# Kernel optimization log

Hardware: AMD Instinct MI355X
Metric: run time of the kernel (lower is better)

Reference implementation:

```python
import jax, jax.numpy as jnp
import numpy as np

N = 524288
MAXV = 8  # rect-rect intersection has at most 8 vertices
EPS = 1e-8


def setup_inputs() -> dict:
    key = jax.random.key(0)
    k1, k2, k3 = jax.random.split(key, 3)
    return {
        "box": jax.random.normal(k1, (N, 11), jnp.float32),
        "box_target": jax.random.normal(k2, (N, 11), jnp.float32),
        "weight": jax.random.uniform(k3, (N, 11), jnp.float32),
        "avg_factor": N // 2,
    }


def decode_box(box):
    # [x,y,z,logW,logL,logH,sin,cos,v...] -> [x,y,z,W,L,H,yaw,v...]
    yaw = jnp.arctan2(box[..., 6], box[..., 7])
    return jnp.concatenate(
        [box[..., :3], jnp.exp(box[..., 3:6]), yaw[..., None], box[..., 8:]], axis=-1)


def get_rect_vertices(bev):
    # bev: (5,) = [cx, cy, w, l, yaw] -> (4, 2) corners, CCW, rotated about center
    cx, cy, w, l, yaw = bev[0], bev[1], bev[2], bev[3], bev[4]
    dx, dy = w / 2, l / 2
    lx = jnp.stack([-dx, dx, dx, -dx])
    ly = jnp.stack([-dy, -dy, dy, dy])
    s, c = jnp.sin(yaw), jnp.cos(yaw)
    return jnp.stack([lx * c - ly * s + cx, lx * s + ly * c + cy], axis=-1)


def clip_halfplane(poly, count, a, b):
    # Sutherland-Hodgman clip of poly (MAXV,2) with `count` valid verts
    # against left side of directed edge a->b. Fixed-size buffer + mask.
    d = b - a  # (2,)
    idx = jnp.arange(MAXV)
    cnt = jnp.maximum(count, 1)
    prev = poly[(idx - 1) % cnt]
    cur = poly

    def is_left(p):
        return d[0] * (p[..., 1] - a[1]) - d[1] * (p[..., 0] - a[0]) >= 0

    cur_in, prev_in = is_left(cur), is_left(prev)
    num = (a[0] - prev[:, 0]) * d[1] - (a[1] - prev[:, 1]) * d[0]
    den = (cur[:, 0] - prev[:, 0]) * d[1] - (cur[:, 1] - prev[:, 1]) * d[0] + EPS
    ip = prev + (num / den)[:, None] * (cur - prev)  # edge/halfplane intersection
    valid = idx < count
    emit_ip = valid & (prev_in ^ cur_in)   # crossing edge -> emit intersection
    emit_cur = valid & cur_in              # inside vertex -> emit it
    # interleave per-input-edge outputs in original order (ip, then cur)
    pts = jnp.stack([ip, cur], axis=1).reshape(2 * MAXV, 2)
    emit = jnp.stack([emit_ip, emit_cur], axis=1).reshape(2 * MAXV)
    pos = jnp.where(emit, jnp.cumsum(emit) - 1, MAXV)  # compact valid pts to front
    out = jnp.zeros((MAXV, 2), poly.dtype).at[pos].set(
        jnp.where(emit[:, None], pts, 0.0), mode="drop")
    return out, jnp.minimum(emit.sum(), MAXV).astype(jnp.int32)


def poly_area(poly, count):
    # shoelace over the `count` valid vertices
    idx = jnp.arange(MAXV)
    nxt = poly[(idx + 1) % jnp.maximum(count, 1)]
    cross = jnp.where(idx < count, poly[:, 0] * nxt[:, 1] - poly[:, 1] * nxt[:, 0], 0.0)
    return jnp.abs(cross.sum() / 2.0)


def giou_one(bev1, bev2):
    v1 = get_rect_vertices(bev1)  # (4,2)
    v2 = get_rect_vertices(bev2)
    poly = jnp.zeros((MAXV, 2), bev1.dtype).at[:4].set(v1)
    count = jnp.int32(4)
    for i in range(4):  # clip subject rect by 4 half-planes of clip rect
        poly, count = clip_halfplane(poly, count, v2[i], v2[(i + 1) % 4])
        count = jnp.where(count < 3, 0, count)  # degenerate -> empty (original break)
    inter = poly_area(poly, count)
    area1 = bev1[2] * bev1[3]
    area2 = bev2[2] * bev2[3]
    union = area1 + area2 - inter
    allp = jnp.concatenate([v1, v2], axis=0)
    enclosing = (allp[:, 0].max() - allp[:, 0].min()) * (allp[:, 1].max() - allp[:, 1].min())
    iou = inter / (union + EPS)
    return iou - (enclosing - union) / (enclosing + EPS)


def _bev(dec):
    return jnp.stack([dec[:, 0], dec[:, 1], dec[:, 3], dec[:, 4], dec[:, 6]], axis=-1)


def reference(box, box_target, weight, avg_factor):
    af = max(float(avg_factor), 1.0)
    # L1 box loss (reg_weights are all 1.0 per init defaults)
    loss_box = (jnp.abs(box - box_target) * weight).sum() / af
    # rotated BEV GIoU loss
    bev_p = _bev(decode_box(box))
    bev_t = _bev(decode_box(box_target))
    giou = jax.vmap(giou_one)(bev_p, bev_t)
    loss_giou = (1.0 - giou).sum() / af
    return loss_box, loss_giou
```

## Files before the change

### kernel.cpp

```cpp
#include <hip/hip_runtime.h>

#define BLOCK 256
#define ITERS 2
#define EPSF 1e-8f

#define CHUNKS 176

struct Nine { float4 b0, b1, b2, t0, t1, t2, w0, w1, w2; };

__device__ __forceinline__ long lmin(long a, long b) { return a < b ? a : b; }

__device__ __forceinline__ float l1c(float4 b, float4 t, float4 w) {
    return fabsf(b.x - t.x) * w.x + fabsf(b.y - t.y) * w.y +
           fabsf(b.z - t.z) * w.z + fabsf(b.w - t.w) * w.w;
}

__device__ __forceinline__ float safe_rcp(float d) {
    float sd = (fabsf(d) > 1e-30f) ? d : copysignf(1e-30f, d);
    return __frcp_rn(sd);
}

__device__ __forceinline__ float clip_len(float px, float py,
                                          float rdx, float rdy,
                                          float hx, float hy) {
    float t1x = (-hx - px) * rdx, t2x = (hx - px) * rdx;
    float t1y = (-hy - py) * rdy, t2y = (hy - py) * rdy;
    float tmin = fmaxf(fmaxf(fminf(t1x, t2x), fminf(t1y, t2y)), 0.f);
    float tmax = fminf(fminf(fmaxf(t1x, t2x), fmaxf(t1y, t2y)), 1.f);
    return fmaxf(tmax - tmin, 0.f);
}

__device__ __forceinline__ float giou_term(
    float cx1, float cy1, float lw1, float ll1, float sy1, float cw1,
    float cx2, float cy2, float lw2, float ll2, float sy2, float cw2)
{
    float w1v = __expf(lw1), l1v = __expf(ll1);
    float w2v = __expf(lw2), l2v = __expf(ll2);
    float r1 = rsqrtf(fmaxf(sy1 * sy1 + cw1 * cw1, 1e-30f));
    float s1 = sy1 * r1, c1 = cw1 * r1;
    float r2 = rsqrtf(fmaxf(sy2 * sy2 + cw2 * cw2, 1e-30f));
    float s2 = sy2 * r2, c2 = cw2 * r2;

    float hx1 = 0.5f * w1v, hy1 = 0.5f * l1v;
    float hx2 = 0.5f * w2v, hy2 = 0.5f * l2v;

    float e1x = fabsf(hx1 * c1) + fabsf(hy1 * s1);
    float e1y = fabsf(hx1 * s1) + fabsf(hy1 * c1);
    float e2x = fabsf(hx2 * c2) + fabsf(hy2 * s2);
    float e2y = fabsf(hx2 * s2) + fabsf(hy2 * c2);
    float enc = (fmaxf(cx1 + e1x, cx2 + e2x) - fminf(cx1 - e1x, cx2 - e2x))
              * (fmaxf(cy1 + e1y, cy2 + e2y) - fminf(cy1 - e1y, cy2 - e2y));

    float dxw = cx1 - cx2, dyw = cy1 - cy2;
    float txl =  c2 * dxw + s2 * dyw;
    float tyl = -s2 * dxw + c2 * dyw;
    float cr_ = c1 * c2 + s1 * s2;
    float sr_ = s1 * c2 - c1 * s2;

    float ax_ = hx1 * cr_, ay_ = hx1 * sr_;
    float bx_ = hy1 * sr_, by_ = hy1 * cr_;
    float q0x = txl - ax_ + bx_, q0y = tyl - ay_ - by_;
    float q1x = txl + ax_ + bx_, q1y = tyl + ay_ - by_;
    float q2x = txl + ax_ - bx_, q2y = tyl + ay_ + by_;
    float q3x = txl - ax_ - bx_, q3y = tyl - ay_ + by_;

    float inter2 = 0.f;
    {
        float d01x = 2.f * ax_, d01y = 2.f * ay_;
        float d12x = -2.f * bx_, d12y = 2.f * by_;
        float r01x = safe_rcp(d01x), r01y = safe_rcp(d01y);
        float r12x = safe_rcp(d12x), r12y = safe_rcp(d12y);
        float L0 = clip_len(q0x, q0y,  r01x,  r01y, hx2, hy2);
        inter2 += L0 * (q0x * d01y - q0y * d01x);
        float L1 = clip_len(q1x, q1y,  r12x,  r12y, hx2, hy2);
        inter2 += L1 * (q1x * d12y - q1y * d12x);
        float L2 = clip_len(q2x, q2y, -r01x, -r01y, hx2, hy2);
        inter2 += L2 * (q2y * d01x - q2x * d01y);
        float L3 = clip_len(q3x, q3y, -r12x, -r12y, hx2, hy2);
        inter2 += L3 * (q3y * d12x - q3x * d12y);
    }
    {
        float zx = -hx2 - txl, zy = -hy2 - tyl;
        float u0x =  cr_ * zx + sr_ * zy;
        float u0y = -sr_ * zx + cr_ * zy;
        float E0x =  2.f * hx2 * cr_, E0y = -2.f * hx2 * sr_;
        float E1x =  2.f * hy2 * sr_, E1y =  2.f * hy2 * cr_;
        float u1x = u0x + E0x, u1y = u0y + E0y;
        float u2x = u1x + E1x, u2y = u1y + E1y;
        float u3x = u0x + E1x, u3y = u0y + E1y;
        float re0x = safe_rcp(E0x), re0y = safe_rcp(E0y);
        float re1x = safe_rcp(E1x), re1y = safe_rcp(E1y);
        float tsum = 0.f;
        tsum += clip_len(u0x, u0y,  re0x,  re0y, hx1, hy1);
        tsum += clip_len(u1x, u1y,  re1x,  re1y, hx1, hy1);
        tsum += clip_len(u2x, u2y, -re0x, -re0y, hx1, hy1);
        tsum += clip_len(u3x, u3y, -re1x, -re1y, hx1, hy1);
        inter2 += 2.f * hx2 * hy2 * tsum;
    }

    float inter = 0.5f * fabsf(inter2);
    float areaU = w1v * l1v + w2v * l2v - inter;
    float iou = inter / (areaU + EPSF);
    float giou = iou - (enc - areaU) / (enc + EPSF);
    return 1.f - giou;
}

__global__ __launch_bounds__(BLOCK) void box_loss_main(
    const float4* __restrict__ b4, const float4* __restrict__ t4,
    const float4* __restrict__ w4, int n, float* __restrict__ partials)
{
    __shared__ float4 lds[4][2][CHUNKS];
    __shared__ float red[8];

    const int tid = threadIdx.x, wv = tid >> 6, lane = tid & 63;
    const long nf  = (long)n * 11;
    const long ncl = (nf >> 2) > 0 ? (nf >> 2) : 1;
    const bool third = lane < 48;

    float sumL1 = 0.f, sumG = 0.f;

    const long base = (long)blockIdx.x * (BLOCK * ITERS) + wv * 64;

    Nine cur, nxt;
    {
        long cb = (base * 11) >> 2;
        long i0 = lmin(cb + lane, ncl - 1);
        long i1 = lmin(cb + lane + 64, ncl - 1);
        long i2 = lmin(cb + (third ? lane : 47) + 128, ncl - 1);
        cur.b0 = b4[i0]; cur.b1 = b4[i1]; cur.b2 = b4[i2];
        cur.t0 = t4[i0]; cur.t1 = t4[i1]; cur.t2 = t4[i2];
        cur.w0 = w4[i0]; cur.w1 = w4[i1]; cur.w2 = w4[i2];
    }

#pragma unroll
    for (int k = 0; k < ITERS; ++k) {
        const long wb = base + (long)k * BLOCK;
        if (k + 1 < ITERS) {
            long cb = ((wb + BLOCK) * 11) >> 2;
            long i0 = lmin(cb + lane, ncl - 1);
            long i1 = lmin(cb + lane + 64, ncl - 1);
            long i2 = lmin(cb + (third ? lane : 47) + 128, ncl - 1);
            nxt.b0 = b4[i0]; nxt.b1 = b4[i1]; nxt.b2 = b4[i2];
            nxt.t0 = t4[i0]; nxt.t1 = t4[i1]; nxt.t2 = t4[i2];
            nxt.w0 = w4[i0]; nxt.w1 = w4[i1]; nxt.w2 = w4[i2];
        }

        const long cb = (wb * 11) >> 2;
        if (cb + lane < ncl)               sumL1 += l1c(cur.b0, cur.t0, cur.w0);
        if (cb + lane + 64 < ncl)          sumL1 += l1c(cur.b1, cur.t1, cur.w1);
        if (third && cb + lane + 128 < ncl) sumL1 += l1c(cur.b2, cur.t2, cur.w2);

        lds[wv][0][lane] = cur.b0; lds[wv][0][lane + 64] = cur.b1;
        if (third) lds[wv][0][lane + 128] = cur.b2;
        lds[wv][1][lane] = cur.t0; lds[wv][1][lane + 64] = cur.t1;
        if (third) lds[wv][1][lane + 128] = cur.t2;

        asm volatile("s_waitcnt lgkmcnt(0)" ::: "memory");
        __builtin_amdgcn_sched_barrier(0);

        const float* rb = (const float*)&lds[wv][0][0] + lane * 11;
        const float* rt = (const float*)&lds[wv][1][0] + lane * 11;
        float g = giou_term(rb[0], rb[1], rb[3], rb[4], rb[6], rb[7],
                            rt[0], rt[1], rt[3], rt[4], rt[6], rt[7]);
        sumG += ((wb + lane) < n) ? g : 0.f;

        if (k + 1 < ITERS) cur = nxt;
    }

#pragma unroll
    for (int off = 32; off > 0; off >>= 1) {
        sumL1 += __shfl_down(sumL1, off);
        sumG  += __shfl_down(sumG, off);
    }
    if (lane == 0) { red[wv] = sumL1; red[4 + wv] = sumG; }
    __syncthreads();
    if (tid == 0) {
        partials[2 * (size_t)blockIdx.x]     = red[0] + red[1] + red[2] + red[3];
        partials[2 * (size_t)blockIdx.x + 1] = red[4] + red[5] + red[6] + red[7];
    }
}

__global__ __launch_bounds__(256) void box_loss_final(
    const float* __restrict__ partials, int nblk,
    const int* __restrict__ avg_factor, float* __restrict__ out)
{
    __shared__ float red[8];
    float a = 0.f, g = 0.f;
    for (int i = threadIdx.x; i < nblk; i += 256) {
        a += partials[2 * (size_t)i];
        g += partials[2 * (size_t)i + 1];
    }
#pragma unroll
    for (int off = 32; off > 0; off >>= 1) {
        a += __shfl_down(a, off);
        g += __shfl_down(g, off);
    }
    const int wave = threadIdx.x >> 6, lane = threadIdx.x & 63;
    if (lane == 0) { red[wave] = a; red[4 + wave] = g; }
    __syncthreads();
    if (threadIdx.x == 0) {
        float af = (float)(*avg_factor);
        if (af < 1.f) af = 1.f;
        out[0] = (red[0] + red[1] + red[2] + red[3]) / af;
        out[1] = (red[4] + red[5] + red[6] + red[7]) / af;
    }
}

extern "C" void kernel_launch(void* const* d_in, const int* in_sizes, int n_in,
                              void* d_out, int out_size, void* d_ws, size_t ws_size,
                              hipStream_t stream) {
    const float4* b4 = (const float4*)d_in[0];
    const float4* t4 = (const float4*)d_in[1];
    const float4* w4 = (const float4*)d_in[2];
    const int*    af = (const int*)d_in[3];
    float* out = (float*)d_out;
    float* partials = (float*)d_ws;

    int n = in_sizes[0] / 11;
    int nblk = (n + BLOCK * ITERS - 1) / (BLOCK * ITERS);
    if (nblk < 1) nblk = 1;

    hipLaunchKernelGGL(box_loss_main, dim3(nblk), dim3(BLOCK), 0, stream,
                       b4, t4, w4, n, partials);
    hipLaunchKernelGGL(box_loss_final, dim3(1), dim3(256), 0, stream,
                       partials, nblk, af, out);
}
```

Baseline: 21.13 us.

## Use single-wave blocks with triple-buffered direct global-to-LDS async loads

Replaces the register double-buffered loads and the explicit LDS stores with global_load_lds DMA into a three-stage LDS ring, so each wave issues loads two rounds ahead and waits with vmcnt counters. Blocks shrink to one wave that processes 12 rounds of 64 boxes each, which removes the cross-wave LDS reduction and the __syncthreads. The intent is deeper memory latency hiding and less VGPR pressure. In exchange the grid is smaller, there are fewer waves per block, and correctness depends on the hand-written vmcnt values matching the number of outstanding loads.

```diff
diff --git a/kernel.cpp b/kernel.cpp
--- a/kernel.cpp
+++ b/kernel.cpp
@@ -1,12 +1,15 @@
 #include <hip/hip_runtime.h>
 
-#define BLOCK 256
-#define ITERS 2
+#define BLOCK 64
+#define ITERS 12
 #define EPSF 1e-8f
 
-#define CHUNKS 176
-
-struct Nine { float4 b0, b1, b2, t0, t1, t2, w0, w1, w2; };
+typedef __attribute__((address_space(3))) void       lds_vp;
+typedef const __attribute__((address_space(1))) void glb_vp;
+
+__device__ __forceinline__ void gll16(const float4* g, float4* l) {
+    __builtin_amdgcn_global_load_lds((glb_vp*)g, (lds_vp*)l, 16, 0, 0);
+}
 
 __device__ __forceinline__ long lmin(long a, long b) { return a < b ? a : b; }
 
@@ -109,62 +112,58 @@
     const float4* __restrict__ b4, const float4* __restrict__ t4,
     const float4* __restrict__ w4, int n, float* __restrict__ partials)
 {
-    __shared__ float4 lds[4][2][CHUNKS];
-    __shared__ float red[8];
-
-    const int tid = threadIdx.x, wv = tid >> 6, lane = tid & 63;
-    const long nf  = (long)n * 11;
-    const long ncl = (nf >> 2) > 0 ? (nf >> 2) : 1;
-    const bool third = lane < 48;
+    __shared__ float4 lds[3][3][192];
+
+    const int  lane = threadIdx.x;
+    const long nf   = (long)n * 11;
+    const long ncl  = (nf >> 2) > 0 ? (nf >> 2) : 1;
+    const long base = (long)blockIdx.x * (ITERS * 64);
+
+    auto stage = [&](int r, int q) {
+        long cb = ((base + (long)r * 64) * 11) >> 2;
+        long c0 = lmin(cb + lane,       ncl - 1);
+        long c1 = lmin(cb + 64  + lane, ncl - 1);
+        long c2 = lmin(cb + 128 + lane, ncl - 1);
+        gll16(b4 + c0, &lds[q][0][0]);
+        gll16(t4 + c0, &lds[q][1][0]);
+        gll16(w4 + c0, &lds[q][2][0]);
+        gll16(b4 + c1, &lds[q][0][64]);
+        gll16(t4 + c1, &lds[q][1][64]);
+        gll16(w4 + c1, &lds[q][2][64]);
+        gll16(b4 + c2, &lds[q][0][128]);
+        gll16(t4 + c2, &lds[q][1][128]);
+        gll16(w4 + c2, &lds[q][2][128]);
+    };
+
+    stage(0, 0);
+    stage(1, 1);
 
     float sumL1 = 0.f, sumG = 0.f;
 
-    const long base = (long)blockIdx.x * (BLOCK * ITERS) + wv * 64;
-
-    Nine cur, nxt;
-    {
-        long cb = (base * 11) >> 2;
-        long i0 = lmin(cb + lane, ncl - 1);
-        long i1 = lmin(cb + lane + 64, ncl - 1);
-        long i2 = lmin(cb + (third ? lane : 47) + 128, ncl - 1);
-        cur.b0 = b4[i0]; cur.b1 = b4[i1]; cur.b2 = b4[i2];
-        cur.t0 = t4[i0]; cur.t1 = t4[i1]; cur.t2 = t4[i2];
-        cur.w0 = w4[i0]; cur.w1 = w4[i1]; cur.w2 = w4[i2];
-    }
-
-#pragma unroll
-    for (int k = 0; k < ITERS; ++k) {
-        const long wb = base + (long)k * BLOCK;
-        if (k + 1 < ITERS) {
-            long cb = ((wb + BLOCK) * 11) >> 2;
-            long i0 = lmin(cb + lane, ncl - 1);
-            long i1 = lmin(cb + lane + 64, ncl - 1);
-            long i2 = lmin(cb + (third ? lane : 47) + 128, ncl - 1);
-            nxt.b0 = b4[i0]; nxt.b1 = b4[i1]; nxt.b2 = b4[i2];
-            nxt.t0 = t4[i0]; nxt.t1 = t4[i1]; nxt.t2 = t4[i2];
-            nxt.w0 = w4[i0]; nxt.w1 = w4[i1]; nxt.w2 = w4[i2];
+    for (int r = 0; r < ITERS; ++r) {
+        const int q = r % 3;
+        if (r + 2 < ITERS) stage(r + 2, (r + 2) % 3);
+
+        if (r + 2 < ITERS)      asm volatile("s_waitcnt vmcnt(18)" ::: "memory");
+        else if (r + 1 < ITERS) asm volatile("s_waitcnt vmcnt(9)"  ::: "memory");
+        else                    asm volatile("s_waitcnt vmcnt(0)"  ::: "memory");
+
+        const long wb = base + (long)r * 64;
+        const long cb = (wb * 11) >> 2;
+
+        if (cb + lane < ncl)
+            sumL1 += l1c(lds[q][0][lane], lds[q][1][lane], lds[q][2][lane]);
+        if (cb + 64 + lane < ncl)
+            sumL1 += l1c(lds[q][0][lane + 64], lds[q][1][lane + 64], lds[q][2][lane + 64]);
+        if (lane < 48 && cb + 128 + lane < ncl)
+            sumL1 += l1c(lds[q][0][lane + 128], lds[q][1][lane + 128], lds[q][2][lane + 128]);
+
+        if (wb + lane < n) {
+            const float* rb = (const float*)&lds[q][0][0] + lane * 11;
+            const float* rt = (const float*)&lds[q][1][0] + lane * 11;
+            sumG += giou_term(rb[0], rb[1], rb[3], rb[4], rb[6], rb[7],
+                              rt[0], rt[1], rt[3], rt[4], rt[6], rt[7]);
         }
-
-        const long cb = (wb * 11) >> 2;
-        if (cb + lane < ncl)               sumL1 += l1c(cur.b0, cur.t0, cur.w0);
-        if (cb + lane + 64 < ncl)          sumL1 += l1c(cur.b1, cur.t1, cur.w1);
-        if (third && cb + lane + 128 < ncl) sumL1 += l1c(cur.b2, cur.t2, cur.w2);
-
-        lds[wv][0][lane] = cur.b0; lds[wv][0][lane + 64] = cur.b1;
-        if (third) lds[wv][0][lane + 128] = cur.b2;
-        lds[wv][1][lane] = cur.t0; lds[wv][1][lane + 64] = cur.t1;
-        if (third) lds[wv][1][lane + 128] = cur.t2;
-
-        asm volatile("s_waitcnt lgkmcnt(0)" ::: "memory");
-        __builtin_amdgcn_sched_barrier(0);
-
-        const float* rb = (const float*)&lds[wv][0][0] + lane * 11;
-        const float* rt = (const float*)&lds[wv][1][0] + lane * 11;
-        float g = giou_term(rb[0], rb[1], rb[3], rb[4], rb[6], rb[7],
-                            rt[0], rt[1], rt[3], rt[4], rt[6], rt[7]);
-        sumG += ((wb + lane) < n) ? g : 0.f;
-
-        if (k + 1 < ITERS) cur = nxt;
     }
 
 #pragma unroll
@@ -172,11 +171,9 @@
         sumL1 += __shfl_down(sumL1, off);
         sumG  += __shfl_down(sumG, off);
     }
-    if (lane == 0) { red[wv] = sumL1; red[4 + wv] = sumG; }
-    __syncthreads();
-    if (tid == 0) {
-        partials[2 * (size_t)blockIdx.x]     = red[0] + red[1] + red[2] + red[3];
-        partials[2 * (size_t)blockIdx.x + 1] = red[4] + red[5] + red[6] + red[7];
+    if (lane == 0) {
+        partials[2 * (size_t)blockIdx.x]     = sumL1;
+        partials[2 * (size_t)blockIdx.x + 1] = sumG;
     }
 }
 
@@ -217,7 +214,8 @@
     float* partials = (float*)d_ws;
 
     int n = in_sizes[0] / 11;
-    int nblk = (n + BLOCK * ITERS - 1) / (BLOCK * ITERS);
+    int per_blk = ITERS * 64;
+    int nblk = (n + per_blk - 1) / per_blk;
     if (nblk < 1) nblk = 1;
 
     hipLaunchKernelGGL(box_loss_main, dim3(nblk), dim3(BLOCK), 0, stream,
```

New measurement: 28.72 us. 1.36x slower.
